# Kernel optimization log

Measured on AMD Instinct MI355X. Metric: run time of the kernel, lower is better.

Reference implementation:

```python
import jax, jax.numpy as jnp
import numpy as np


def setup_inputs() -> dict:
    key = jax.random.key(0)
    k1, k2 = jax.random.split(key)
    B, H, W, P, C = 8, 256, 256, 200, 20
    prototype_activations = jax.random.normal(k1, (B, H * W, P), dtype=jnp.float32)
    # labels in 0..C; forward subtracts 1, so 0 becomes -1 (ignored)
    target_labels = jax.random.randint(k2, (B, H, W), 0, C + 1).astype(jnp.int64)
    # 10 prototypes per class, block-diagonal one-hot identity [P, C]
    proto_cls = jnp.repeat(jnp.arange(C), P // C)
    prototype_class_identity = jax.nn.one_hot(proto_cls, C, dtype=jnp.float32)
    return {
        "prototype_activations": prototype_activations,
        "target_labels": target_labels,
        "prototype_class_identity": prototype_class_identity,
    }


def reference(prototype_activations, target_labels, prototype_class_identity):
    # norm_type == 'l1' (init kwarg)
    B = target_labels.shape[0]
    labels = target_labels.reshape(B, -1).astype(jnp.int32) - 1          # [B, N]
    P, C = prototype_class_identity.shape
    A = prototype_activations.reshape(B, -1, P)                           # [B, N, P]
    N = labels.shape[1]

    valid_px = (labels >= 0) & (labels < C)                               # [B, N]
    # per-image segment ids; invalid pixels go to sentinel slot C
    seg = jnp.where(valid_px, labels, C) + jnp.arange(B)[:, None] * (C + 1)
    seg = seg.reshape(-1)                                                 # [B*N]
    nseg = B * (C + 1)

    abs_a = jnp.abs(A).reshape(B * N, P)
    # sum of |activation| per (image, class) per prototype -> [B, C, P]
    sums = jax.ops.segment_sum(abs_a, seg, num_segments=nseg).reshape(B, C + 1, P)[:, :C]
    counts = jax.ops.segment_sum(jnp.ones((B * N,), A.dtype), seg, num_segments=nseg)
    counts = counts.reshape(B, C + 1)[:, :C]                              # [B, C] pixel counts

    proto_count = prototype_class_identity.sum(axis=0)                    # [C]
    # l1: per-prototype norm = sum|act| / n_pixels; then mean over class prototypes
    per_proto = sums / jnp.maximum(counts, 1.0)[:, :, None]               # [B, C, P]
    class_norm = jnp.einsum('bcp,pc->bc', per_proto, prototype_class_identity)
    class_norm = class_norm / jnp.maximum(proto_count, 1.0)               # [B, C]

    valid_cls = (counts > 0) & (proto_count > 0)                          # [B, C]
    num = jnp.sum(jnp.where(valid_cls, class_norm, 0.0))
    den = jnp.maximum(jnp.sum(valid_cls), 1).astype(class_norm.dtype)
    return num / den
```

## Files before the change

### kernel.cpp

```cpp
#include <hip/hip_runtime.h>
#include <math.h>

constexpr int B = 8;
constexpr int N = 256 * 256;
constexpr int P = 200;
constexpr int C = 20;
constexpr int NSLOT = B * C;
constexpr int MAXNNZ = P * C;

__global__ __launch_bounds__(256) void setup_kernel(
    const float* __restrict__ ident,
    float* __restrict__ ws_acc,
    int* __restrict__ ws_off,
    int* __restrict__ ws_idx,
    float* __restrict__ ws_w) {
  __shared__ int cnts[C];
  __shared__ int soff[C + 1];
  const int t = threadIdx.x;

  for (int i = t; i < 2 * NSLOT; i += blockDim.x) ws_acc[i] = 0.0f;

  if (t < C) {
    int c = 0;
    for (int p = 0; p < P; ++p)
      if (ident[p * C + t] != 0.0f) ++c;
    cnts[t] = c;
  }
  __syncthreads();
  if (t == 0) {
    int acc = 0;
    for (int c = 0; c < C; ++c) { soff[c] = acc; acc += cnts[c]; }
    soff[C] = acc;
  }
  __syncthreads();
  if (t <= C) ws_off[t] = soff[t];
  if (t < C) {
    int o = soff[t];
    for (int p = 0; p < P; ++p) {
      float v = ident[p * C + t];
      if (v != 0.0f) { ws_idx[o] = p; ws_w[o] = v; ++o; }
    }
  }
}

__global__ __launch_bounds__(256) void main_kernel(
    const float* __restrict__ A,
    const int* __restrict__ labels,
    const int* __restrict__ ws_off,
    const int* __restrict__ ws_idx,
    const float* __restrict__ ws_w,
    float* __restrict__ ws_acc) {
  __shared__ float s_sum[NSLOT];
  __shared__ float s_cnt[NSLOT];
  __shared__ int s_off[C + 1];
  __shared__ int s_idx[MAXNNZ];
  __shared__ float s_w[MAXNNZ];

  const int t = threadIdx.x;
  for (int i = t; i < NSLOT; i += blockDim.x) { s_sum[i] = 0.0f; s_cnt[i] = 0.0f; }
  for (int i = t; i <= C; i += blockDim.x) s_off[i] = ws_off[i];
  __syncthreads();
  const int total = s_off[C];
  for (int i = t; i < total; i += blockDim.x) { s_idx[i] = ws_idx[i]; s_w[i] = ws_w[i]; }
  __syncthreads();

  const long long NP = (long long)B * N;
  const long long stride = (long long)gridDim.x * blockDim.x;
  for (long long i = (long long)blockIdx.x * blockDim.x + t; i < NP; i += stride) {
    const int lab = labels[i] - 1;
    if (lab >= 0 && lab < C) {
      const float* row = A + (size_t)i * P;
      const int o0 = s_off[lab];
      const int o1 = s_off[lab + 1];
      float s = 0.0f;
      #pragma unroll 2
      for (int k = o0; k < o1; ++k) s += fabsf(row[s_idx[k]]) * s_w[k];
      const int b = (int)(i / N);
      const int slot = b * C + lab;
      atomicAdd(&s_sum[slot], s);
      atomicAdd(&s_cnt[slot], 1.0f);
    }
  }
  __syncthreads();
  for (int i = t; i < NSLOT; i += blockDim.x) {
    const float cv = s_cnt[i];
    if (cv != 0.0f) {
      atomicAdd(&ws_acc[i], s_sum[i]);
      atomicAdd(&ws_acc[NSLOT + i], cv);
    }
  }
}

__global__ __launch_bounds__(256) void final_kernel(
    const float* __restrict__ ident,
    const float* __restrict__ ws_acc,
    float* __restrict__ out) {
  __shared__ float pc[C];
  __shared__ float red_num[256];
  __shared__ float red_den[256];
  const int t = threadIdx.x;
  if (t < C) {
    float s = 0.0f;
    for (int p = 0; p < P; ++p) s += ident[p * C + t];
    pc[t] = s;
  }
  __syncthreads();
  float num = 0.0f, den = 0.0f;
  for (int i = t; i < NSLOT; i += blockDim.x) {
    const float cnt = ws_acc[NSLOT + i];
    const float p = pc[i % C];
    if (cnt > 0.0f && p > 0.0f) {
      num += ws_acc[i] / fmaxf(cnt, 1.0f) / fmaxf(p, 1.0f);
      den += 1.0f;
    }
  }
  red_num[t] = num;
  red_den[t] = den;
  __syncthreads();
  for (int s = 128; s > 0; s >>= 1) {
    if (t < s) { red_num[t] += red_num[t + s]; red_den[t] += red_den[t + s]; }
    __syncthreads();
  }
  if (t == 0) out[0] = red_num[0] / fmaxf(red_den[0], 1.0f);
}

extern "C" void kernel_launch(void* const* d_in, const int* in_sizes, int n_in,
                              void* d_out, int out_size, void* d_ws, size_t ws_size,
                              hipStream_t stream) {
  const float* A      = (const float*)d_in[0];
  const int*   labels = (const int*)d_in[1];
  const float* ident  = (const float*)d_in[2];
  float* out = (float*)d_out;

  float* ws_acc = (float*)d_ws;
  int*   ws_off = (int*)(ws_acc + 2 * NSLOT);
  int*   ws_idx = ws_off + (C + 1);
  float* ws_w   = (float*)(ws_idx + MAXNNZ);

  setup_kernel<<<1, 256, 0, stream>>>(ident, ws_acc, ws_off, ws_idx, ws_w);
  main_kernel<<<512, 256, 0, stream>>>(A, labels, ws_off, ws_idx, ws_w, ws_acc);
  final_kernel<<<1, 256, 0, stream>>>(ident, ws_acc, out);
}
```

Before: 534.9 us.

## Add contiguous-run fast path with float2 loads and enlarge grid

```diff
diff --git a/kernel.cpp b/kernel.cpp
--- a/kernel.cpp
+++ b/kernel.cpp
@@ -1,5 +1,6 @@
 #include <hip/hip_runtime.h>
 #include <math.h>
+#include <stdint.h>
 
 constexpr int B = 8;
 constexpr int N = 256 * 256;
@@ -13,24 +14,40 @@
     float* __restrict__ ws_acc,
     int* __restrict__ ws_off,
     int* __restrict__ ws_idx,
-    float* __restrict__ ws_w) {
+    float* __restrict__ ws_w,
+    int* __restrict__ ws_start,
+    int* __restrict__ ws_cnt,
+    int* __restrict__ ws_flag) {
   __shared__ int cnts[C];
   __shared__ int soff[C + 1];
+  __shared__ int okcls[C];
   const int t = threadIdx.x;
 
   for (int i = t; i < 2 * NSLOT; i += blockDim.x) ws_acc[i] = 0.0f;
 
   if (t < C) {
-    int c = 0;
-    for (int p = 0; p < P; ++p)
-      if (ident[p * C + t] != 0.0f) ++c;
-    cnts[t] = c;
+    int cnt = 0, first = -1, last = -1, uniform = 1;
+    for (int p = 0; p < P; ++p) {
+      float v = ident[p * C + t];
+      if (v != 0.0f) {
+        if (first < 0) first = p;
+        last = p;
+        ++cnt;
+        if (v != 1.0f) uniform = 0;
+      }
+    }
+    cnts[t] = cnt;
+    const int contig = (cnt == 0) || (last - first + 1 == cnt);
+    okcls[t] = (contig && uniform) ? 1 : 0;
+    ws_start[t] = (first < 0) ? 0 : first;
+    ws_cnt[t] = cnt;
   }
   __syncthreads();
   if (t == 0) {
-    int acc = 0;
-    for (int c = 0; c < C; ++c) { soff[c] = acc; acc += cnts[c]; }
+    int acc = 0, ok = 1;
+    for (int c = 0; c < C; ++c) { soff[c] = acc; acc += cnts[c]; ok &= okcls[c]; }
     soff[C] = acc;
+    ws_flag[0] = ok;
   }
   __syncthreads();
   if (t <= C) ws_off[t] = soff[t];
@@ -49,34 +66,55 @@
     const int* __restrict__ ws_off,
     const int* __restrict__ ws_idx,
     const float* __restrict__ ws_w,
+    const int* __restrict__ ws_start,
+    const int* __restrict__ ws_cnt,
+    const int* __restrict__ ws_flag,
     float* __restrict__ ws_acc) {
   __shared__ float s_sum[NSLOT];
   __shared__ float s_cnt[NSLOT];
+  __shared__ int s_start[C];
+  __shared__ int s_len[C];
   __shared__ int s_off[C + 1];
   __shared__ int s_idx[MAXNNZ];
   __shared__ float s_w[MAXNNZ];
 
   const int t = threadIdx.x;
   for (int i = t; i < NSLOT; i += blockDim.x) { s_sum[i] = 0.0f; s_cnt[i] = 0.0f; }
+  if (t < C) { s_start[t] = ws_start[t]; s_len[t] = ws_cnt[t]; }
   for (int i = t; i <= C; i += blockDim.x) s_off[i] = ws_off[i];
   __syncthreads();
+  const int fast = ws_flag[0];
   const int total = s_off[C];
-  for (int i = t; i < total; i += blockDim.x) { s_idx[i] = ws_idx[i]; s_w[i] = ws_w[i]; }
+  if (!fast) {
+    for (int i = t; i < total; i += blockDim.x) { s_idx[i] = ws_idx[i]; s_w[i] = ws_w[i]; }
+  }
   __syncthreads();
 
-  const long long NP = (long long)B * N;
-  const long long stride = (long long)gridDim.x * blockDim.x;
-  for (long long i = (long long)blockIdx.x * blockDim.x + t; i < NP; i += stride) {
+  const int NP = B * N;
+  const int stride = gridDim.x * blockDim.x;
+  for (int i = blockIdx.x * blockDim.x + t; i < NP; i += stride) {
     const int lab = labels[i] - 1;
     if (lab >= 0 && lab < C) {
       const float* row = A + (size_t)i * P;
-      const int o0 = s_off[lab];
-      const int o1 = s_off[lab + 1];
       float s = 0.0f;
-      #pragma unroll 2
-      for (int k = o0; k < o1; ++k) s += fabsf(row[s_idx[k]]) * s_w[k];
-      const int b = (int)(i / N);
-      const int slot = b * C + lab;
+      if (fast) {
+        const int p0 = s_start[lab];
+        const int cnt = s_len[lab];
+        const float* base = row + p0;
+        int k = 0;
+        if ((p0 & 1) && k < cnt) { s += fabsf(base[k]); ++k; }
+        #pragma unroll 5
+        for (; k + 1 < cnt; k += 2) {
+          const float2 v = *(const float2*)(base + k);
+          s += fabsf(v.x) + fabsf(v.y);
+        }
+        if (k < cnt) s += fabsf(base[k]);
+      } else {
+        const int o0 = s_off[lab];
+        const int o1 = s_off[lab + 1];
+        for (int k = o0; k < o1; ++k) s += fabsf(row[s_idx[k]]) * s_w[k];
+      }
+      const int slot = (i >> 16) * C + lab;
       atomicAdd(&s_sum[slot], s);
       atomicAdd(&s_cnt[slot], 1.0f);
     }
@@ -132,12 +170,17 @@
   const float* ident  = (const float*)d_in[2];
   float* out = (float*)d_out;
 
-  float* ws_acc = (float*)d_ws;
-  int*   ws_off = (int*)(ws_acc + 2 * NSLOT);
-  int*   ws_idx = ws_off + (C + 1);
-  float* ws_w   = (float*)(ws_idx + MAXNNZ);
+  float* ws_acc   = (float*)d_ws;
+  int*   ws_off   = (int*)(ws_acc + 2 * NSLOT);
+  int*   ws_idx   = ws_off + (C + 1);
+  float* ws_w     = (float*)(ws_idx + MAXNNZ);
+  int*   ws_start = (int*)(ws_w + MAXNNZ);
+  int*   ws_cnt   = ws_start + C;
+  int*   ws_flag  = ws_cnt + C;
 
-  setup_kernel<<<1, 256, 0, stream>>>(ident, ws_acc, ws_off, ws_idx, ws_w);
-  main_kernel<<<512, 256, 0, stream>>>(A, labels, ws_off, ws_idx, ws_w, ws_acc);
+  setup_kernel<<<1, 256, 0, stream>>>(ident, ws_acc, ws_off, ws_idx, ws_w,
+                                      ws_start, ws_cnt, ws_flag);
+  main_kernel<<<2048, 256, 0, stream>>>(A, labels, ws_off, ws_idx, ws_w,
+                                        ws_start, ws_cnt, ws_flag, ws_acc);
   final_kernel<<<1, 256, 0, stream>>>(ident, ws_acc, out);
 }
```

New measurement: 572.3 us. +7.0%, slower.

## Fuse main and final kernels with last-block ticket; contiguous float2 fast path

Applied to the files above, without the earlier changes.

```diff
diff --git a/kernel.cpp b/kernel.cpp
--- a/kernel.cpp
+++ b/kernel.cpp
@@ -6,111 +6,121 @@
 constexpr int P = 200;
 constexpr int C = 20;
 constexpr int NSLOT = B * C;
-constexpr int MAXNNZ = P * C;
+constexpr int GRID = (B * N) / 256;
 
-__global__ __launch_bounds__(256) void setup_kernel(
+__global__ __launch_bounds__(256) void zero_kernel(float* __restrict__ ws_acc,
+                                                   int* __restrict__ done) {
+  const int t = threadIdx.x;
+  for (int i = t; i < 2 * NSLOT; i += 256) ws_acc[i] = 0.0f;
+  if (t == 0) *done = 0;
+}
+
+__global__ __launch_bounds__(256) void fused_kernel(
+    const float* __restrict__ A,
+    const int* __restrict__ labels,
     const float* __restrict__ ident,
     float* __restrict__ ws_acc,
-    int* __restrict__ ws_off,
-    int* __restrict__ ws_idx,
-    float* __restrict__ ws_w) {
-  __shared__ int cnts[C];
-  __shared__ int soff[C + 1];
+    int* __restrict__ done,
+    float* __restrict__ out) {
+  __shared__ float s_sum[NSLOT];
+  __shared__ float s_cnt[NSLOT];
+  __shared__ int s_start[C];
+  __shared__ int s_len[C];
+  __shared__ int s_okc[C];
+  __shared__ int s_fast;
+  __shared__ int s_ticket;
+  __shared__ float s_pc[C];
+  __shared__ float red_num[256];
+  __shared__ float red_den[256];
+
   const int t = threadIdx.x;
-
-  for (int i = t; i < 2 * NSLOT; i += blockDim.x) ws_acc[i] = 0.0f;
+  for (int i = t; i < NSLOT; i += 256) { s_sum[i] = 0.0f; s_cnt[i] = 0.0f; }
 
   if (t < C) {
-    int c = 0;
-    for (int p = 0; p < P; ++p)
-      if (ident[p * C + t] != 0.0f) ++c;
-    cnts[t] = c;
+    int cnt = 0, first = -1, last = -1, uniform = 1;
+    for (int p = 0; p < P; ++p) {
+      const float v = ident[p * C + t];
+      if (v != 0.0f) {
+        if (first < 0) first = p;
+        last = p;
+        ++cnt;
+        if (v != 1.0f) uniform = 0;
+      }
+    }
+    s_start[t] = (first < 0) ? 0 : first;
+    s_len[t] = cnt;
+    s_okc[t] = (cnt == 0) || (uniform && (last - first + 1 == cnt));
   }
   __syncthreads();
   if (t == 0) {
-    int acc = 0;
-    for (int c = 0; c < C; ++c) { soff[c] = acc; acc += cnts[c]; }
-    soff[C] = acc;
+    int ok = 1;
+    for (int c = 0; c < C; ++c) ok &= s_okc[c];
+    s_fast = ok;
   }
   __syncthreads();
-  if (t <= C) ws_off[t] = soff[t];
-  if (t < C) {
-    int o = soff[t];
-    for (int p = 0; p < P; ++p) {
-      float v = ident[p * C + t];
-      if (v != 0.0f) { ws_idx[o] = p; ws_w[o] = v; ++o; }
-    }
-  }
-}
+  const int fast = s_fast;
 
-__global__ __launch_bounds__(256) void main_kernel(
-    const float* __restrict__ A,
-    const int* __restrict__ labels,
-    const int* __restrict__ ws_off,
-    const int* __restrict__ ws_idx,
-    const float* __restrict__ ws_w,
-    float* __restrict__ ws_acc) {
-  __shared__ float s_sum[NSLOT];
-  __shared__ float s_cnt[NSLOT];
-  __shared__ int s_off[C + 1];
-  __shared__ int s_idx[MAXNNZ];
-  __shared__ float s_w[MAXNNZ];
-
-  const int t = threadIdx.x;
-  for (int i = t; i < NSLOT; i += blockDim.x) { s_sum[i] = 0.0f; s_cnt[i] = 0.0f; }
-  for (int i = t; i <= C; i += blockDim.x) s_off[i] = ws_off[i];
-  __syncthreads();
-  const int total = s_off[C];
-  for (int i = t; i < total; i += blockDim.x) { s_idx[i] = ws_idx[i]; s_w[i] = ws_w[i]; }
-  __syncthreads();
-
-  const long long NP = (long long)B * N;
-  const long long stride = (long long)gridDim.x * blockDim.x;
-  for (long long i = (long long)blockIdx.x * blockDim.x + t; i < NP; i += stride) {
+  const int i = blockIdx.x * 256 + t;
+  if (i < B * N) {
     const int lab = labels[i] - 1;
     if (lab >= 0 && lab < C) {
-      const float* row = A + (size_t)i * P;
-      const int o0 = s_off[lab];
-      const int o1 = s_off[lab + 1];
       float s = 0.0f;
-      #pragma unroll 2
-      for (int k = o0; k < o1; ++k) s += fabsf(row[s_idx[k]]) * s_w[k];
-      const int b = (int)(i / N);
-      const int slot = b * C + lab;
+      if (fast) {
+        const int p0 = s_start[lab];
+        const int cnt = s_len[lab];
+        const float* base = A + (size_t)i * P + p0;
+        int k = 0;
+        if ((p0 & 1) && k < cnt) { s += fabsf(base[k]); ++k; }
+        #pragma unroll 5
+        for (; k + 1 < cnt; k += 2) {
+          const float2 v = *(const float2*)(base + k);
+          s += fabsf(v.x) + fabsf(v.y);
+        }
+        if (k < cnt) s += fabsf(base[k]);
+      } else {
+        const float* row = A + (size_t)i * P;
+        for (int p = 0; p < P; ++p) {
+          const float w = ident[p * C + lab];
+          if (w != 0.0f) s += fabsf(row[p]) * w;
+        }
+      }
+      const int slot = (i / N) * C + lab;
       atomicAdd(&s_sum[slot], s);
       atomicAdd(&s_cnt[slot], 1.0f);
     }
   }
   __syncthreads();
-  for (int i = t; i < NSLOT; i += blockDim.x) {
-    const float cv = s_cnt[i];
+
+  for (int j = t; j < NSLOT; j += 256) {
+    const float cv = s_cnt[j];
     if (cv != 0.0f) {
-      atomicAdd(&ws_acc[i], s_sum[i]);
-      atomicAdd(&ws_acc[NSLOT + i], cv);
+      atomicAdd(&ws_acc[j], s_sum[j]);
+      atomicAdd(&ws_acc[NSLOT + j], cv);
     }
   }
-}
 
-__global__ __launch_bounds__(256) void final_kernel(
-    const float* __restrict__ ident,
-    const float* __restrict__ ws_acc,
-    float* __restrict__ out) {
-  __shared__ float pc[C];
-  __shared__ float red_num[256];
-  __shared__ float red_den[256];
-  const int t = threadIdx.x;
+  __threadfence();
+  __syncthreads();
+  if (t == 0) s_ticket = atomicAdd(done, 1);
+  __syncthreads();
+  if (s_ticket != (int)gridDim.x - 1) return;
+
+  __threadfence();
   if (t < C) {
     float s = 0.0f;
     for (int p = 0; p < P; ++p) s += ident[p * C + t];
-    pc[t] = s;
+    s_pc[t] = s;
   }
   __syncthreads();
   float num = 0.0f, den = 0.0f;
-  for (int i = t; i < NSLOT; i += blockDim.x) {
-    const float cnt = ws_acc[NSLOT + i];
-    const float p = pc[i % C];
+  for (int j = t; j < NSLOT; j += 256) {
+    const float cnt = __hip_atomic_load(&ws_acc[NSLOT + j], __ATOMIC_RELAXED,
+                                        __HIP_MEMORY_SCOPE_AGENT);
+    const float sm = __hip_atomic_load(&ws_acc[j], __ATOMIC_RELAXED,
+                                       __HIP_MEMORY_SCOPE_AGENT);
+    const float p = s_pc[j % C];
     if (cnt > 0.0f && p > 0.0f) {
-      num += ws_acc[i] / fmaxf(cnt, 1.0f) / fmaxf(p, 1.0f);
+      num += sm / fmaxf(cnt, 1.0f) / fmaxf(p, 1.0f);
       den += 1.0f;
     }
   }
@@ -133,11 +143,8 @@
   float* out = (float*)d_out;
 
   float* ws_acc = (float*)d_ws;
-  int*   ws_off = (int*)(ws_acc + 2 * NSLOT);
-  int*   ws_idx = ws_off + (C + 1);
-  float* ws_w   = (float*)(ws_idx + MAXNNZ);
+  int*   done   = (int*)(ws_acc + 2 * NSLOT);
 
-  setup_kernel<<<1, 256, 0, stream>>>(ident, ws_acc, ws_off, ws_idx, ws_w);
-  main_kernel<<<512, 256, 0, stream>>>(A, labels, ws_off, ws_idx, ws_w, ws_acc);
-  final_kernel<<<1, 256, 0, stream>>>(ident, ws_acc, out);
+  zero_kernel<<<1, 256, 0, stream>>>(ws_acc, done);
+  fused_kernel<<<GRID, 256, 0, stream>>>(A, labels, ident, ws_acc, done, out);
 }
```

New measurement: 805.6 us. +50.6%, slower.
